# Kernel optimization log

Hardware: AMD Instinct MI355X
Metric: run time of the kernel (lower is better)

## Reference

```python
import jax, jax.numpy as jnp
import numpy as np

K_SIZE = 3            # kernel_size
PAD = K_SIZE // 2     # zero padding on each side
EPS = 1e-5            # torch layer_norm default eps


def setup_inputs() -> dict:
    key = jax.random.key(0)
    ks = jax.random.split(key, 9)
    B, C, H, W = 4, 256, 64, 64
    Cout = 256
    sc = 1.0 / np.sqrt(C)
    return {
        "x":  jax.random.normal(ks[0], (B, C, H, W), dtype=jnp.float32),
        "Wq": jax.random.normal(ks[1], (C, C), dtype=jnp.float32) * sc,
        "bq": jax.random.normal(ks[2], (C,), dtype=jnp.float32) * 0.02,
        "Wk": jax.random.normal(ks[3], (C, C), dtype=jnp.float32) * sc,
        "bk": jax.random.normal(ks[4], (C,), dtype=jnp.float32) * 0.02,
        "Wv": jax.random.normal(ks[5], (C, C), dtype=jnp.float32) * sc,
        "bv": jax.random.normal(ks[6], (C,), dtype=jnp.float32) * 0.02,
        "Wo": jax.random.normal(ks[7], (C, Cout), dtype=jnp.float32) * sc,
        "bo": jax.random.normal(ks[8], (Cout,), dtype=jnp.float32) * 0.02,
    }


def _forward(x, Wq, bq, Wk, bk, Wv, bv, Wo, bo):
    B, C, H, W = x.shape
    # F.layer_norm(x, [H, W]): normalize over last two dims per (b, c), no affine
    mean = jnp.mean(x, axis=(2, 3), keepdims=True)
    var = jnp.var(x, axis=(2, 3), keepdims=True)
    xn = (x - mean) * jax.lax.rsqrt(var + EPS)
    # zero pad spatial dims
    p = jnp.pad(xn, ((0, 0), (0, 0), (PAD, PAD), (PAD, PAD)))
    # channels-last for per-pixel linears
    p = jnp.transpose(p, (0, 2, 3, 1))          # [B, Hp, Wp, C]
    xc = jnp.transpose(xn, (0, 2, 3, 1))        # [B, H,  W,  C] (window centers)
    scale = jnp.asarray(C, x.dtype) ** -0.5     # depth_scale = C**-0.5
    q = (xc @ Wq + bq) * scale                  # [B, H, W, C] (center-token query)
    kf = p @ Wk + bk                            # [B, Hp, Wp, C]
    vf = p @ Wv + bv
    # gather the kk=9 shifted views -> window tokens per pixel
    Kw = jnp.stack([kf[:, dh:dh + H, dw:dw + W, :]
                    for dh in range(K_SIZE) for dw in range(K_SIZE)], axis=3)  # [B,H,W,kk,C]
    Vw = jnp.stack([vf[:, dh:dh + H, dw:dw + W, :]
                    for dh in range(K_SIZE) for dw in range(K_SIZE)], axis=3)
    logits = jnp.einsum('bhwc,bhwnc->bhwn', q, Kw)     # [B, H, W, kk]
    attn = jax.nn.softmax(logits, axis=-1)
    ctx = jnp.einsum('bhwn,bhwnc->bhwc', attn, Vw)     # [B, H, W, C]
    out = ctx @ Wo + bo                                # [B, H, W, Cout]
    return jnp.transpose(out, (0, 3, 1, 2))            # [B, Cout, H, W]


def reference(x, Wq, bq, Wk, bk, Wv, bv, Wo, bo):
    return _forward(x, Wq, bq, Wk, bk, Wv, bv, Wo, bo)
```

## Files before the change

### kernel.cpp

```cpp
#include <hip/hip_runtime.h>
#include <hip/hip_bf16.h>
#include <stdint.h>

typedef __bf16 bf16x8 __attribute__((ext_vector_type(8)));
typedef float f32x4 __attribute__((ext_vector_type(4)));

#define KDIM 256
#define MB 4608
#define MTOT 18432
#define QKVS 768

__device__ __forceinline__ float b2f(ushort u){
    union { float f; uint32_t i; } x; x.i = ((uint32_t)u) << 16; return x.f;
}
__device__ __forceinline__ ushort f2b(float f){
    uint32_t u = __float_as_uint(f);
    uint32_t r = (u + 0x7fffu + ((u >> 16) & 1u)) >> 16;
    return (ushort)r;
}

__global__ __launch_bounds__(256)
void ln_fuse(const float* __restrict__ x, ushort* __restrict__ xt,
             float* __restrict__ psum, float* __restrict__ psum2){
    __shared__ ushort sh[128 * 68];
    __shared__ float ssum[16 * 132], ssum2[16 * 132];
    const int bid = blockIdx.x;
    const int b = bid >> 7, rem = bid & 127, h = rem >> 1, ch = (rem & 1) * 128;
    const int tid = threadIdx.x;
    const int csub = tid >> 4, w4 = tid & 15;
#pragma unroll
    for (int i = 0; i < 8; ++i){
        int c = csub + 16 * i;
        float4 v = *(const float4*)(x + ((size_t)(b * 256 + ch + c)) * 4096
                                      + h * 64 + w4 * 4);
        ushort4 u; u.x = f2b(v.x); u.y = f2b(v.y); u.z = f2b(v.z); u.w = f2b(v.w);
        *(ushort4*)&sh[c * 68 + w4 * 4] = u;
        ssum [w4 * 132 + c] = v.x + v.y + v.z + v.w;
        ssum2[w4 * 132 + c] = v.x * v.x + v.y * v.y + v.z * v.z + v.w * v.w;
    }
    __syncthreads();
    if (tid < 128){
        float S = 0.f, S2 = 0.f;
#pragma unroll
        for (int j = 0; j < 16; ++j){ S += ssum[j * 132 + tid]; S2 += ssum2[j * 132 + tid]; }
        psum [(b * 64 + h) * 256 + ch + tid] = S;
        psum2[(b * 64 + h) * 256 + ch + tid] = S2;
    }
    const int c16 = tid & 15, w16 = tid >> 4;
#pragma unroll
    for (int p = 0; p < 4; ++p){
        int w = p * 16 + w16;
        union { ushort u[8]; uint4 v; } r;
#pragma unroll
        for (int j = 0; j < 8; ++j) r.u[j] = sh[(c16 * 8 + j) * 68 + w];
        size_t row = (size_t)b * MB + (size_t)(h + 1) * 66 + (w + 1);
        *(uint4*)(xt + row * 256 + ch + c16 * 8) = r.v;
    }
}

__global__ __launch_bounds__(256)
void prep2(const float* __restrict__ Wq, const float* __restrict__ bq,
           const float* __restrict__ Wk, const float* __restrict__ bk,
           const float* __restrict__ Wv, const float* __restrict__ bv,
           const float* __restrict__ Wo,
           const float* __restrict__ psum, const float* __restrict__ psum2,
           ushort* __restrict__ wtq, ushort* __restrict__ wot,
           float* __restrict__ biasp, ushort* __restrict__ xt){
    __shared__ float shW[32 * 33];
    __shared__ float shS[8 * 32], shS2[8 * 32], shRV[4 * 32], shM[256];
    const int bid = blockIdx.x, tid = threadIdx.x;
    if (bid < 192){
        int mat = bid / 64, tile = bid % 64;
        int ti = tile & 7, tj = tile >> 3;
        {
            int kk = tid & 31, idx = tid >> 5;
            int b = idx >> 1, h0 = (idx & 1) * 32;
            float S = 0.f, S2 = 0.f;
            for (int r = 0; r < 32; ++r){
                int off = (b * 64 + h0 + r) * 256 + tj * 32 + kk;
                S += psum[off]; S2 += psum2[off];
            }
            shS[idx * 32 + kk] = S; shS2[idx * 32 + kk] = S2;
        }
        __syncthreads();
        if (tid < 128){
            int b = tid >> 5, kk = tid & 31;
            float S  = shS [(b * 2) * 32 + kk] + shS [(b * 2 + 1) * 32 + kk];
            float S2 = shS2[(b * 2) * 32 + kk] + shS2[(b * 2 + 1) * 32 + kk];
            float m = S * (1.f / 4096.f);
            float v = S2 * (1.f / 4096.f) - m * m;
            shRV[b * 32 + kk] = rsqrtf(v + 1e-5f);
        }
        const float* src = (mat == 0) ? Wq : (mat == 1) ? Wk : Wv;
        float qs = (mat == 0) ? 0.0625f : 1.0f;
        int tx = tid & 31, ty = tid >> 5;
#pragma unroll
        for (int i = 0; i < 4; ++i)
            shW[(ty + i * 8) * 33 + tx] =
                src[(size_t)(tj * 32 + ty + i * 8) * 256 + ti * 32 + tx] * qs;
        __syncthreads();
#pragma unroll
        for (int b = 0; b < 4; ++b){
            float rv = shRV[b * 32 + tx];
#pragma unroll
            for (int i = 0; i < 4; ++i){
                int n = mat * 256 + ti * 32 + ty + i * 8;
                wtq[((size_t)b * 768 + n) * 256 + tj * 32 + tx] =
                    f2b(shW[tx * 33 + ty + i * 8] * rv);
            }
        }
    } else if (bid < 256){
        int tile = bid - 192;
        int ti = tile & 7, tj = tile >> 3;
        int tx = tid & 31, ty = tid >> 5;
#pragma unroll
        for (int i = 0; i < 4; ++i)
            shW[(ty + i * 8) * 33 + tx] =
                Wo[(size_t)(tj * 32 + ty + i * 8) * 256 + ti * 32 + tx];
        __syncthreads();
#pragma unroll
        for (int i = 0; i < 4; ++i)
            wot[(size_t)(ti * 32 + ty + i * 8) * 256 + tj * 32 + tx] =
                f2b(shW[tx * 33 + ty + i * 8]);
    } else if (bid < 268){
        int t = bid - 256;
        int b = t / 3, mat = t % 3;
        float S = 0.f, S2 = 0.f;
        for (int h = 0; h < 64; ++h){
            S += psum[(b * 64 + h) * 256 + tid]; S2 += psum2[(b * 64 + h) * 256 + tid];
        }
        float m = S * (1.f / 4096.f);
        float v = S2 * (1.f / 4096.f) - m * m;
        shM[tid] = m * rsqrtf(v + 1e-5f);
        __syncthreads();
        const float* W  = (mat == 0) ? Wq : (mat == 1) ? Wk : Wv;
        const float* bb = (mat == 0) ? bq : (mat == 1) ? bk : bv;
        float qs = (mat == 0) ? 0.0625f : 1.0f;
        float acc = 0.f;
        for (int c = 0; c < 256; ++c)
            acc += shM[c] * W[(size_t)c * 256 + tid];
        biasp[b * 768 + mat * 256 + tid] = (bb[tid] - acc) * qs;
    } else {
        int t = bid - 268;
        int b = t / 16, seg = t % 16;
        float S = 0.f;
        for (int h = 0; h < 64; ++h) S += psum[(b * 64 + h) * 256 + tid];
        ushort mb = f2b(S * (1.f / 4096.f));
        for (int r = 0; r < 32; ++r){
            int j = seg * 32 + r;
            int row;
            if (j < 260){
                int h66, w66;
                if (j < 66)       { h66 = 0;       w66 = j; }
                else if (j < 132) { h66 = 65;      w66 = j - 66; }
                else if (j < 196) { h66 = j - 131; w66 = 0; }
                else              { h66 = j - 195; w66 = 65; }
                row = h66 * 66 + w66;
            } else row = 4356 + (j - 260);
            xt[((size_t)b * MB + row) * 256 + tid] = mb;
        }
    }
}

__global__ __launch_bounds__(512, 1)
void gemm_qkv(const ushort* __restrict__ X, const ushort* __restrict__ Y,
              const float* __restrict__ bias, ushort* __restrict__ zb){
    __shared__ ushort ldsA[2][256 * 64];
    __shared__ ushort ldsB[2][256 * 64];
    const int tid  = threadIdx.x;
    const int lane = tid & 63;
    const int wid  = tid >> 6;
    const int wm   = wid >> 2;
    const int wn   = wid & 3;
    const int id    = blockIdx.x;
    const int mtile = id % 72, ntile = id / 72;
    const int x0 = mtile * 256, y0 = ntile * 256;
    const int bsel = x0 / MB;
    const ushort* Yb   = Y + ((size_t)bsel * QKVS + y0) * 256;
    const float* biasb = bias + bsel * 768;

    auto stage = [&](int buf, int k0){
#pragma unroll
        for (int i = 0; i < 4; ++i){
            int f   = i * 512 + tid;
            int row = f >> 3, cp = f & 7;
            int cs  = cp ^ (row & 7);
            const ushort* ga = X  + (size_t)(x0 + row) * KDIM + k0 + cs * 8;
            const ushort* gb = Yb + (size_t)row        * KDIM + k0 + cs * 8;
            __builtin_amdgcn_global_load_lds(
                (const __attribute__((address_space(1))) void*)ga,
                (__attribute__((address_space(3))) void*)&ldsA[buf][f * 8], 16, 0, 0);
            __builtin_amdgcn_global_load_lds(
                (const __attribute__((address_space(1))) void*)gb,
                (__attribute__((address_space(3))) void*)&ldsB[buf][f * 8], 16, 0, 0);
        }
    };

    f32x4 acc[8][4];
#pragma unroll
    for (int i = 0; i < 8; ++i)
#pragma unroll
        for (int j = 0; j < 4; ++j) acc[i][j] = f32x4{0.f, 0.f, 0.f, 0.f};

    stage(0, 0);
    stage(1, 64);
#pragma unroll
    for (int t = 0; t < 4; ++t){
        if (t < 3) asm volatile("s_waitcnt vmcnt(8)" ::: "memory");
        else       asm volatile("s_waitcnt vmcnt(0)" ::: "memory");
        __builtin_amdgcn_sched_barrier(0);
        __builtin_amdgcn_s_barrier();
        __builtin_amdgcn_sched_barrier(0);
        const int buf = t & 1;
        __builtin_amdgcn_s_setprio(1);
#pragma unroll
        for (int kk = 0; kk < 2; ++kk){
            bf16x8 af[8], bf[4];
#pragma unroll
            for (int fm = 0; fm < 8; ++fm){
                int r = wm * 128 + fm * 16 + (lane & 15);
                int c = kk * 4 + (lane >> 4);
                af[fm] = *(const bf16x8*)&ldsA[buf][(r * 8 + (c ^ (r & 7))) * 8];
            }
#pragma unroll
            for (int fn = 0; fn < 4; ++fn){
                int r = wn * 64 + fn * 16 + (lane & 15);
                int c = kk * 4 + (lane >> 4);
                bf[fn] = *(const bf16x8*)&ldsB[buf][(r * 8 + (c ^ (r & 7))) * 8];
            }
#pragma unroll
            for (int fm = 0; fm < 8; ++fm)
#pragma unroll
                for (int fn = 0; fn < 4; ++fn)
                    acc[fm][fn] = __builtin_amdgcn_mfma_f32_16x16x32_bf16(
                        af[fm], bf[fn], acc[fm][fn], 0, 0, 0);
        }
        __builtin_amdgcn_s_setprio(0);
        __builtin_amdgcn_sched_barrier(0);
        __builtin_amdgcn_s_barrier();
        __builtin_amdgcn_sched_barrier(0);
        if (t < 2) stage(t & 1, (t + 2) * 64);
    }

#pragma unroll
    for (int fm = 0; fm < 8; ++fm){
#pragma unroll
        for (int fn = 0; fn < 4; ++fn){
            int xr = x0 + wm * 128 + fm * 16 + ((lane >> 4) << 2);
            int yc = y0 + wn * 64 + fn * 16 + (lane & 15);
            float bv = biasb[yc];
#pragma unroll
            for (int r = 0; r < 4; ++r)
                zb[(size_t)(xr + r) * QKVS + yc] = f2b(acc[fm][fn][r] + bv);
        }
    }
}

__global__ __launch_bounds__(256, 2)
void gemm_out(const ushort* __restrict__ X, const ushort* __restrict__ Y,
              const float* __restrict__ bias, float* __restrict__ zf){
    __shared__ ushort ldsX[2][128 * 64];
    __shared__ ushort ldsY[2][128 * 64];
    const int tid  = threadIdx.x;
    const int lane = tid & 63;
    const int wid  = tid >> 6;
    const int wm   = wid >> 1, wn = wid & 1;
    const int x0   = blockIdx.x * 128, y0 = blockIdx.y * 128;

    auto stage = [&](int buf, int k0){
#pragma unroll
        for (int i = 0; i < 4; ++i){
            int f   = i * 256 + tid;
            int row = f >> 3, cp = f & 7;
            int cs  = cp ^ (row & 7);
            const ushort* gx = X + (size_t)(x0 + row) * KDIM + k0 + cs * 8;
            const ushort* gy = Y + (size_t)(y0 + row) * KDIM + k0 + cs * 8;
            __builtin_amdgcn_global_load_lds(
                (const __attribute__((address_space(1))) void*)gx,
                (__attribute__((address_space(3))) void*)&ldsX[buf][f * 8], 16, 0, 0);
            __builtin_amdgcn_global_load_lds(
                (const __attribute__((address_space(1))) void*)gy,
                (__attribute__((address_space(3))) void*)&ldsY[buf][f * 8], 16, 0, 0);
        }
    };

    f32x4 acc[4][4];
#pragma unroll
    for (int i = 0; i < 4; ++i)
#pragma unroll
        for (int j = 0; j < 4; ++j) acc[i][j] = f32x4{0.f, 0.f, 0.f, 0.f};

    stage(0, 0);
    int buf = 0;
    for (int t = 0; t < 4; ++t){
        __syncthreads();
        if (t < 3) stage(buf ^ 1, (t + 1) * 64);
#pragma unroll
        for (int kk = 0; kk < 2; ++kk){
            bf16x8 xa[4], yb[4];
#pragma unroll
            for (int fm = 0; fm < 4; ++fm){
                int r = wm * 64 + fm * 16 + (lane & 15);
                int c = kk * 4 + (lane >> 4);
                xa[fm] = *(const bf16x8*)&ldsX[buf][(r * 8 + (c ^ (r & 7))) * 8];
            }
#pragma unroll
            for (int fn = 0; fn < 4; ++fn){
                int r = wn * 64 + fn * 16 + (lane & 15);
                int c = kk * 4 + (lane >> 4);
                yb[fn] = *(const bf16x8*)&ldsY[buf][(r * 8 + (c ^ (r & 7))) * 8];
            }
#pragma unroll
            for (int fm = 0; fm < 4; ++fm)
#pragma unroll
                for (int fn = 0; fn < 4; ++fn)
                    acc[fm][fn] = __builtin_amdgcn_mfma_f32_16x16x32_bf16(
                        xa[fm], yb[fn], acc[fm][fn], 0, 0, 0);
        }
        buf ^= 1;
    }

#pragma unroll
    for (int fm = 0; fm < 4; ++fm){
#pragma unroll
        for (int fn = 0; fn < 4; ++fn){
            int xr = x0 + wm * 64 + fm * 16 + ((lane >> 4) << 2);
            int yc = y0 + wn * 64 + fn * 16 + (lane & 15);
            int bpix = yc >> 12, hw = yc & 4095;
#pragma unroll
            for (int r = 0; r < 4; ++r){
                int ch = xr + r;
                zf[((size_t)(bpix * 256 + ch)) * 4096 + hw] =
                    acc[fm][fn][r] + bias[ch];
            }
        }
    }
}

__global__ __launch_bounds__(256)
void attn_win(const ushort* __restrict__ qkv, ushort* __restrict__ ctx){
    int pix  = blockIdx.x * 4 + (threadIdx.x >> 6);
    int lane = threadIdx.x & 63;
    int b = pix >> 12, hw = pix & 4095;
    int h = hw >> 6, w = hw & 63;
    size_t base = (size_t)b * MB;
    size_t crow = base + (size_t)(h + 1) * 66 + (w + 1);

    ushort4 q4 = *(const ushort4*)(qkv + crow * QKVS + lane * 4);
    float q0 = b2f(q4.x), q1 = b2f(q4.y), q2 = b2f(q4.z), q3 = b2f(q4.w);

    float lg[9];
    size_t rows[9];
#pragma unroll
    for (int n = 0; n < 9; ++n){
        int dh = n / 3, dw = n % 3;
        size_t row = base + (size_t)(h + dh) * 66 + (w + dw);
        rows[n] = row;
        ushort4 k4 = *(const ushort4*)(qkv + row * QKVS + 256 + lane * 4);
        float d = q0 * b2f(k4.x) + q1 * b2f(k4.y) + q2 * b2f(k4.z) + q3 * b2f(k4.w);
#pragma unroll
        for (int off = 32; off; off >>= 1) d += __shfl_xor(d, off);
        lg[n] = d;
    }
    float m = lg[0];
#pragma unroll
    for (int n = 1; n < 9; ++n) m = fmaxf(m, lg[n]);
    float e[9], s = 0.f;
#pragma unroll
    for (int n = 0; n < 9; ++n){ e[n] = __expf(lg[n] - m); s += e[n]; }
    float inv = 1.f / s;

    float c0 = 0.f, c1 = 0.f, c2 = 0.f, c3 = 0.f;
#pragma unroll
    for (int n = 0; n < 9; ++n){
        float a = e[n] * inv;
        ushort4 v4 = *(const ushort4*)(qkv + rows[n] * QKVS + 512 + lane * 4);
        c0 += a * b2f(v4.x); c1 += a * b2f(v4.y);
        c2 += a * b2f(v4.z); c3 += a * b2f(v4.w);
    }
    ushort4 o; o.x = f2b(c0); o.y = f2b(c1); o.z = f2b(c2); o.w = f2b(c3);
    *(ushort4*)(ctx + (size_t)pix * 256 + lane * 4) = o;
}

extern "C" void kernel_launch(void* const* d_in, const int* in_sizes, int n_in,
                              void* d_out, int out_size, void* d_ws, size_t ws_size,
                              hipStream_t stream){
    const float* x  = (const float*)d_in[0];
    const float* Wq = (const float*)d_in[1];
    const float* bq = (const float*)d_in[2];
    const float* Wk = (const float*)d_in[3];
    const float* bk = (const float*)d_in[4];
    const float* Wv = (const float*)d_in[5];
    const float* bv = (const float*)d_in[6];
    const float* Wo = (const float*)d_in[7];
    const float* bo = (const float*)d_in[8];
    float* out = (float*)d_out;

    char* ws = (char*)d_ws;
    ushort* wtq    = (ushort*)(ws);
    ushort* wot    = (ushort*)(ws + 1572864);
    float*  biasp  = (float*) (ws + 1703936);
    float*  psum   = (float*) (ws + 1716224);
    float*  psum2  = (float*) (ws + 1978368);
    ushort* xt     = (ushort*)(ws + 2240512);
    ushort* qkv    = (ushort*)(ws + 11677696);
    ushort* ctx    = (ushort*)(ws + 39989248);

    ln_fuse<<<512, 256, 0, stream>>>(x, xt, psum, psum2);
    prep2<<<332, 256, 0, stream>>>(Wq, bq, Wk, bk, Wv, bv, Wo,
                                   psum, psum2, wtq, wot, biasp, xt);

    gemm_qkv<<<216, 512, 0, stream>>>(xt, wtq, biasp, qkv);

    attn_win<<<4096, 256, 0, stream>>>(qkv, ctx);

    dim3 g2(2, 128);
    gemm_out<<<g2, 256, 0, stream>>>(wot, ctx, bo, out);
}
```

Before: 59.28 us.

## Fuse windowed attention with output projection GEMM per image row

Merges the attention kernel and the output-projection GEMM into one kernel. Each block handles one image row: it computes 64 pixels of context into LDS and then multiplies by Wo straight from global memory, writing the NCHW output. This drops the ctx round trip through global memory and one launch. In exchange the grid shrinks to 256 blocks of 512 threads, and the Wo operand is no longer staged through LDS.

```diff
diff --git a/kernel.cpp b/kernel.cpp
--- a/kernel.cpp
+++ b/kernel.cpp
@@ -256,130 +256,96 @@
     }
 }
 
-__global__ __launch_bounds__(256, 2)
-void gemm_out(const ushort* __restrict__ X, const ushort* __restrict__ Y,
-              const float* __restrict__ bias, float* __restrict__ zf){
-    __shared__ ushort ldsX[2][128 * 64];
-    __shared__ ushort ldsY[2][128 * 64];
-    const int tid  = threadIdx.x;
-    const int lane = tid & 63;
-    const int wid  = tid >> 6;
-    const int wm   = wid >> 1, wn = wid & 1;
-    const int x0   = blockIdx.x * 128, y0 = blockIdx.y * 128;
-
-    auto stage = [&](int buf, int k0){
-#pragma unroll
-        for (int i = 0; i < 4; ++i){
-            int f   = i * 256 + tid;
-            int row = f >> 3, cp = f & 7;
-            int cs  = cp ^ (row & 7);
-            const ushort* gx = X + (size_t)(x0 + row) * KDIM + k0 + cs * 8;
-            const ushort* gy = Y + (size_t)(y0 + row) * KDIM + k0 + cs * 8;
-            __builtin_amdgcn_global_load_lds(
-                (const __attribute__((address_space(1))) void*)gx,
-                (__attribute__((address_space(3))) void*)&ldsX[buf][f * 8], 16, 0, 0);
-            __builtin_amdgcn_global_load_lds(
-                (const __attribute__((address_space(1))) void*)gy,
-                (__attribute__((address_space(3))) void*)&ldsY[buf][f * 8], 16, 0, 0);
-        }
-    };
-
-    f32x4 acc[4][4];
-#pragma unroll
-    for (int i = 0; i < 4; ++i)
-#pragma unroll
-        for (int j = 0; j < 4; ++j) acc[i][j] = f32x4{0.f, 0.f, 0.f, 0.f};
-
-    stage(0, 0);
-    int buf = 0;
-    for (int t = 0; t < 4; ++t){
-        __syncthreads();
-        if (t < 3) stage(buf ^ 1, (t + 1) * 64);
-#pragma unroll
-        for (int kk = 0; kk < 2; ++kk){
-            bf16x8 xa[4], yb[4];
-#pragma unroll
-            for (int fm = 0; fm < 4; ++fm){
-                int r = wm * 64 + fm * 16 + (lane & 15);
-                int c = kk * 4 + (lane >> 4);
-                xa[fm] = *(const bf16x8*)&ldsX[buf][(r * 8 + (c ^ (r & 7))) * 8];
-            }
-#pragma unroll
-            for (int fn = 0; fn < 4; ++fn){
-                int r = wn * 64 + fn * 16 + (lane & 15);
-                int c = kk * 4 + (lane >> 4);
-                yb[fn] = *(const bf16x8*)&ldsY[buf][(r * 8 + (c ^ (r & 7))) * 8];
-            }
-#pragma unroll
-            for (int fm = 0; fm < 4; ++fm)
-#pragma unroll
-                for (int fn = 0; fn < 4; ++fn)
-                    acc[fm][fn] = __builtin_amdgcn_mfma_f32_16x16x32_bf16(
-                        xa[fm], yb[fn], acc[fm][fn], 0, 0, 0);
-        }
-        buf ^= 1;
+__global__ __launch_bounds__(512, 1)
+void attn_out(const ushort* __restrict__ qkv, const ushort* __restrict__ wot,
+              const float* __restrict__ bo, float* __restrict__ out){
+    __shared__ ushort ctx[64 * 256];
+    const int tid = threadIdx.x, lane = tid & 63, wid = tid >> 6;
+    const int b = blockIdx.x >> 6, h = blockIdx.x & 63;
+    const uint base = (uint)b * MB;
+
+#pragma unroll 1
+    for (int j = 0; j < 8; ++j){
+        const int w = wid * 8 + j;
+        uint crow = base + (uint)(h + 1) * 66 + (w + 1);
+        ushort4 q4 = *(const ushort4*)(qkv + (size_t)crow * QKVS + lane * 4);
+        float q0 = b2f(q4.x), q1 = b2f(q4.y), q2 = b2f(q4.z), q3 = b2f(q4.w);
+
+        float lg[9];
+        uint rows[9];
+#pragma unroll
+        for (int n = 0; n < 9; ++n){
+            int dh = n / 3, dw = n % 3;
+            uint row = base + (uint)(h + dh) * 66 + (w + dw);
+            rows[n] = row;
+            ushort4 k4 = *(const ushort4*)(qkv + (size_t)row * QKVS + 256 + lane * 4);
+            float d = q0 * b2f(k4.x) + q1 * b2f(k4.y) + q2 * b2f(k4.z) + q3 * b2f(k4.w);
+#pragma unroll
+            for (int off = 32; off; off >>= 1) d += __shfl_xor(d, off);
+            lg[n] = d;
+        }
+        float m = lg[0];
+#pragma unroll
+        for (int n = 1; n < 9; ++n) m = fmaxf(m, lg[n]);
+        float e[9], s = 0.f;
+#pragma unroll
+        for (int n = 0; n < 9; ++n){ e[n] = __expf(lg[n] - m); s += e[n]; }
+        float inv = 1.f / s;
+
+        float c0 = 0.f, c1 = 0.f, c2 = 0.f, c3 = 0.f;
+#pragma unroll
+        for (int n = 0; n < 9; ++n){
+            float a = e[n] * inv;
+            ushort4 v4 = *(const ushort4*)(qkv + (size_t)rows[n] * QKVS + 512 + lane * 4);
+            c0 += a * b2f(v4.x); c1 += a * b2f(v4.y);
+            c2 += a * b2f(v4.z); c3 += a * b2f(v4.w);
+        }
+        ushort4 o; o.x = f2b(c0); o.y = f2b(c1); o.z = f2b(c2); o.w = f2b(c3);
+        *(ushort4*)&ctx[w * 256 + (((lane >> 1) ^ (w & 7)) * 8) + (lane & 1) * 4] = o;
+    }
+    __syncthreads();
+
+    const int wmi = wid >> 1, wni = wid & 1;
+    f32x4 acc[4][2];
+#pragma unroll
+    for (int i = 0; i < 4; ++i){ acc[i][0] = f32x4{0,0,0,0}; acc[i][1] = f32x4{0,0,0,0}; }
+
+#pragma unroll
+    for (int kk = 0; kk < 8; ++kk){
+        bf16x8 af[4], bf[2];
+        const int c = kk * 4 + (lane >> 4);
+#pragma unroll
+        for (int fm = 0; fm < 4; ++fm){
+            int r = wmi * 64 + fm * 16 + (lane & 15);
+            af[fm] = *(const bf16x8*)(wot + (size_t)r * 256 + c * 8);
+        }
+#pragma unroll
+        for (int fn = 0; fn < 2; ++fn){
+            int p = wni * 32 + fn * 16 + (lane & 15);
+            bf[fn] = *(const bf16x8*)&ctx[p * 256 + (c ^ (p & 7)) * 8];
+        }
+#pragma unroll
+        for (int fm = 0; fm < 4; ++fm)
+#pragma unroll
+            for (int fn = 0; fn < 2; ++fn)
+                acc[fm][fn] = __builtin_amdgcn_mfma_f32_16x16x32_bf16(
+                    af[fm], bf[fn], acc[fm][fn], 0, 0, 0);
     }
 
 #pragma unroll
     for (int fm = 0; fm < 4; ++fm){
 #pragma unroll
-        for (int fn = 0; fn < 4; ++fn){
-            int xr = x0 + wm * 64 + fm * 16 + ((lane >> 4) << 2);
-            int yc = y0 + wn * 64 + fn * 16 + (lane & 15);
-            int bpix = yc >> 12, hw = yc & 4095;
+        for (int fn = 0; fn < 2; ++fn){
+            int ch0  = wmi * 64 + fm * 16 + ((lane >> 4) << 2);
+            int wpix = wni * 32 + fn * 16 + (lane & 15);
 #pragma unroll
             for (int r = 0; r < 4; ++r){
-                int ch = xr + r;
-                zf[((size_t)(bpix * 256 + ch)) * 4096 + hw] =
-                    acc[fm][fn][r] + bias[ch];
-            }
-        }
-    }
-}
-
-__global__ __launch_bounds__(256)
-void attn_win(const ushort* __restrict__ qkv, ushort* __restrict__ ctx){
-    int pix  = blockIdx.x * 4 + (threadIdx.x >> 6);
-    int lane = threadIdx.x & 63;
-    int b = pix >> 12, hw = pix & 4095;
-    int h = hw >> 6, w = hw & 63;
-    size_t base = (size_t)b * MB;
-    size_t crow = base + (size_t)(h + 1) * 66 + (w + 1);
-
-    ushort4 q4 = *(const ushort4*)(qkv + crow * QKVS + lane * 4);
-    float q0 = b2f(q4.x), q1 = b2f(q4.y), q2 = b2f(q4.z), q3 = b2f(q4.w);
-
-    float lg[9];
-    size_t rows[9];
-#pragma unroll
-    for (int n = 0; n < 9; ++n){
-        int dh = n / 3, dw = n % 3;
-        size_t row = base + (size_t)(h + dh) * 66 + (w + dw);
-        rows[n] = row;
-        ushort4 k4 = *(const ushort4*)(qkv + row * QKVS + 256 + lane * 4);
-        float d = q0 * b2f(k4.x) + q1 * b2f(k4.y) + q2 * b2f(k4.z) + q3 * b2f(k4.w);
-#pragma unroll
-        for (int off = 32; off; off >>= 1) d += __shfl_xor(d, off);
-        lg[n] = d;
-    }
-    float m = lg[0];
-#pragma unroll
-    for (int n = 1; n < 9; ++n) m = fmaxf(m, lg[n]);
-    float e[9], s = 0.f;
-#pragma unroll
-    for (int n = 0; n < 9; ++n){ e[n] = __expf(lg[n] - m); s += e[n]; }
-    float inv = 1.f / s;
-
-    float c0 = 0.f, c1 = 0.f, c2 = 0.f, c3 = 0.f;
-#pragma unroll
-    for (int n = 0; n < 9; ++n){
-        float a = e[n] * inv;
-        ushort4 v4 = *(const ushort4*)(qkv + rows[n] * QKVS + 512 + lane * 4);
-        c0 += a * b2f(v4.x); c1 += a * b2f(v4.y);
-        c2 += a * b2f(v4.z); c3 += a * b2f(v4.w);
-    }
-    ushort4 o; o.x = f2b(c0); o.y = f2b(c1); o.z = f2b(c2); o.w = f2b(c3);
-    *(ushort4*)(ctx + (size_t)pix * 256 + lane * 4) = o;
+                int ch = ch0 + r;
+                out[((size_t)(b * 256 + ch)) * 4096 + h * 64 + wpix] =
+                    acc[fm][fn][r] + bo[ch];
+            }
+        }
+    }
 }
 
 extern "C" void kernel_launch(void* const* d_in, const int* in_sizes, int n_in,
@@ -404,7 +370,6 @@
     float*  psum2  = (float*) (ws + 1978368);
     ushort* xt     = (ushort*)(ws + 2240512);
     ushort* qkv    = (ushort*)(ws + 11677696);
-    ushort* ctx    = (ushort*)(ws + 39989248);
 
     ln_fuse<<<512, 256, 0, stream>>>(x, xt, psum, psum2);
     prep2<<<332, 256, 0, stream>>>(Wq, bq, Wk, bk, Wv, bv, Wo,
@@ -412,8 +377,5 @@
 
     gemm_qkv<<<216, 512, 0, stream>>>(xt, wtq, biasp, qkv);
 
-    attn_win<<<4096, 256, 0, stream>>>(qkv, ctx);
-
-    dim3 g2(2, 128);
-    gemm_out<<<g2, 256, 0, stream>>>(wot, ctx, bo, out);
-}
+    attn_out<<<256, 512, 0, stream>>>(qkv, wot, bo, out);
+}
```

New measurement: 82.06 us. 1.38x slower.

## Drop padded pixel layout; handle window borders via shared pad row

Applied to the files above, without the earlier changes.

The normalized input is now stored unpadded (16384 rows instead of 18432), so the QKV GEMM skips the padded border rows. Out-of-bounds window neighbours in the attention kernel point at a single extra row holding the K/V values a padded pixel would produce: bias only, which is exact because the input is mean-centered before the weight product. The QKV GEMM is also retiled from 256x256 tiles with 512 threads to 128x128 tiles with 256 threads and two blocks per CU. Its hand-tuned waitcnt/setprio pipeline is replaced by a simpler __syncthreads double buffer, which may expose more load latency.

```diff
diff --git a/kernel.cpp b/kernel.cpp
--- a/kernel.cpp
+++ b/kernel.cpp
@@ -6,8 +6,7 @@
 typedef float f32x4 __attribute__((ext_vector_type(4)));
 
 #define KDIM 256
-#define MB 4608
-#define MTOT 18432
+#define NPIX 16384
 #define QKVS 768
 
 __device__ __forceinline__ float b2f(ushort u){
@@ -53,7 +52,7 @@
         union { ushort u[8]; uint4 v; } r;
 #pragma unroll
         for (int j = 0; j < 8; ++j) r.u[j] = sh[(c16 * 8 + j) * 68 + w];
-        size_t row = (size_t)b * MB + (size_t)(h + 1) * 66 + (w + 1);
+        size_t row = (size_t)(b * 4096 + h * 64 + w);
         *(uint4*)(xt + row * 256 + ch + c16 * 8) = r.v;
     }
 }
@@ -65,7 +64,7 @@
            const float* __restrict__ Wo,
            const float* __restrict__ psum, const float* __restrict__ psum2,
            ushort* __restrict__ wtq, ushort* __restrict__ wot,
-           float* __restrict__ biasp, ushort* __restrict__ xt){
+           float* __restrict__ biasp, ushort* __restrict__ qkv){
     __shared__ float shW[32 * 33];
     __shared__ float shS[8 * 32], shS2[8 * 32], shRV[4 * 32], shM[256];
     const int bid = blockIdx.x, tid = threadIdx.x;
@@ -141,112 +140,85 @@
             acc += shM[c] * W[(size_t)c * 256 + tid];
         biasp[b * 768 + mat * 256 + tid] = (bb[tid] - acc) * qs;
     } else {
-        int t = bid - 268;
-        int b = t / 16, seg = t % 16;
-        float S = 0.f;
-        for (int h = 0; h < 64; ++h) S += psum[(b * 64 + h) * 256 + tid];
-        ushort mb = f2b(S * (1.f / 4096.f));
-        for (int r = 0; r < 32; ++r){
-            int j = seg * 32 + r;
-            int row;
-            if (j < 260){
-                int h66, w66;
-                if (j < 66)       { h66 = 0;       w66 = j; }
-                else if (j < 132) { h66 = 65;      w66 = j - 66; }
-                else if (j < 196) { h66 = j - 131; w66 = 0; }
-                else              { h66 = j - 195; w66 = 65; }
-                row = h66 * 66 + w66;
-            } else row = 4356 + (j - 260);
-            xt[((size_t)b * MB + row) * 256 + tid] = mb;
-        }
-    }
-}
-
-__global__ __launch_bounds__(512, 1)
+        ushort* pad = qkv + (size_t)NPIX * QKVS;
+        pad[tid]       = 0;
+        pad[256 + tid] = f2b(bk[tid]);
+        pad[512 + tid] = f2b(bv[tid]);
+    }
+}
+
+__global__ __launch_bounds__(256, 2)
 void gemm_qkv(const ushort* __restrict__ X, const ushort* __restrict__ Y,
               const float* __restrict__ bias, ushort* __restrict__ zb){
-    __shared__ ushort ldsA[2][256 * 64];
-    __shared__ ushort ldsB[2][256 * 64];
+    __shared__ ushort ldsX[2][128 * 64];
+    __shared__ ushort ldsY[2][128 * 64];
     const int tid  = threadIdx.x;
     const int lane = tid & 63;
     const int wid  = tid >> 6;
-    const int wm   = wid >> 2;
-    const int wn   = wid & 3;
-    const int id    = blockIdx.x;
-    const int mtile = id % 72, ntile = id / 72;
-    const int x0 = mtile * 256, y0 = ntile * 256;
-    const int bsel = x0 / MB;
-    const ushort* Yb   = Y + ((size_t)bsel * QKVS + y0) * 256;
-    const float* biasb = bias + bsel * 768;
+    const int wm   = wid >> 1, wn = wid & 1;
+    const int x0   = blockIdx.x * 128, y0 = blockIdx.y * 128;
+    const int bsel = x0 >> 12;
+    const ushort* Yb   = Y + (size_t)bsel * QKVS * 256;
+    const float* biasb = bias + bsel * QKVS;
 
     auto stage = [&](int buf, int k0){
 #pragma unroll
         for (int i = 0; i < 4; ++i){
-            int f   = i * 512 + tid;
+            int f   = i * 256 + tid;
             int row = f >> 3, cp = f & 7;
             int cs  = cp ^ (row & 7);
-            const ushort* ga = X  + (size_t)(x0 + row) * KDIM + k0 + cs * 8;
-            const ushort* gb = Yb + (size_t)row        * KDIM + k0 + cs * 8;
+            const ushort* gx = X  + (size_t)(x0 + row) * KDIM + k0 + cs * 8;
+            const ushort* gy = Yb + (size_t)(y0 + row) * KDIM + k0 + cs * 8;
             __builtin_amdgcn_global_load_lds(
-                (const __attribute__((address_space(1))) void*)ga,
-                (__attribute__((address_space(3))) void*)&ldsA[buf][f * 8], 16, 0, 0);
+                (const __attribute__((address_space(1))) void*)gx,
+                (__attribute__((address_space(3))) void*)&ldsX[buf][f * 8], 16, 0, 0);
             __builtin_amdgcn_global_load_lds(
-                (const __attribute__((address_space(1))) void*)gb,
-                (__attribute__((address_space(3))) void*)&ldsB[buf][f * 8], 16, 0, 0);
+                (const __attribute__((address_space(1))) void*)gy,
+                (__attribute__((address_space(3))) void*)&ldsY[buf][f * 8], 16, 0, 0);
         }
     };
 
-    f32x4 acc[8][4];
-#pragma unroll
-    for (int i = 0; i < 8; ++i)
+    f32x4 acc[4][4];
+#pragma unroll
+    for (int i = 0; i < 4; ++i)
 #pragma unroll
         for (int j = 0; j < 4; ++j) acc[i][j] = f32x4{0.f, 0.f, 0.f, 0.f};
 
     stage(0, 0);
-    stage(1, 64);
-#pragma unroll
+    int buf = 0;
     for (int t = 0; t < 4; ++t){
-        if (t < 3) asm volatile("s_waitcnt vmcnt(8)" ::: "memory");
-        else       asm volatile("s_waitcnt vmcnt(0)" ::: "memory");
-        __builtin_amdgcn_sched_barrier(0);
-        __builtin_amdgcn_s_barrier();
-        __builtin_amdgcn_sched_barrier(0);
-        const int buf = t & 1;
-        __builtin_amdgcn_s_setprio(1);
+        __syncthreads();
+        if (t < 3) stage(buf ^ 1, (t + 1) * 64);
 #pragma unroll
         for (int kk = 0; kk < 2; ++kk){
-            bf16x8 af[8], bf[4];
-#pragma unroll
-            for (int fm = 0; fm < 8; ++fm){
-                int r = wm * 128 + fm * 16 + (lane & 15);
+            bf16x8 xa[4], yb[4];
+#pragma unroll
+            for (int fm = 0; fm < 4; ++fm){
+                int r = wm * 64 + fm * 16 + (lane & 15);
                 int c = kk * 4 + (lane >> 4);
-                af[fm] = *(const bf16x8*)&ldsA[buf][(r * 8 + (c ^ (r & 7))) * 8];
+                xa[fm] = *(const bf16x8*)&ldsX[buf][(r * 8 + (c ^ (r & 7))) * 8];
             }
 #pragma unroll
             for (int fn = 0; fn < 4; ++fn){
                 int r = wn * 64 + fn * 16 + (lane & 15);
                 int c = kk * 4 + (lane >> 4);
-                bf[fn] = *(const bf16x8*)&ldsB[buf][(r * 8 + (c ^ (r & 7))) * 8];
-            }
-#pragma unroll
-            for (int fm = 0; fm < 8; ++fm)
+                yb[fn] = *(const bf16x8*)&ldsY[buf][(r * 8 + (c ^ (r & 7))) * 8];
+            }
+#pragma unroll
+            for (int fm = 0; fm < 4; ++fm)
 #pragma unroll
                 for (int fn = 0; fn < 4; ++fn)
                     acc[fm][fn] = __builtin_amdgcn_mfma_f32_16x16x32_bf16(
-                        af[fm], bf[fn], acc[fm][fn], 0, 0, 0);
-        }
-        __builtin_amdgcn_s_setprio(0);
-        __builtin_amdgcn_sched_barrier(0);
-        __builtin_amdgcn_s_barrier();
-        __builtin_amdgcn_sched_barrier(0);
-        if (t < 2) stage(t & 1, (t + 2) * 64);
-    }
-
-#pragma unroll
-    for (int fm = 0; fm < 8; ++fm){
+                        xa[fm], yb[fn], acc[fm][fn], 0, 0, 0);
+        }
+        buf ^= 1;
+    }
+
+#pragma unroll
+    for (int fm = 0; fm < 4; ++fm){
 #pragma unroll
         for (int fn = 0; fn < 4; ++fn){
-            int xr = x0 + wm * 128 + fm * 16 + ((lane >> 4) << 2);
+            int xr = x0 + wm * 64 + fm * 16 + ((lane >> 4) << 2);
             int yc = y0 + wn * 64 + fn * 16 + (lane & 15);
             float bv = biasb[yc];
 #pragma unroll
@@ -254,6 +226,50 @@
                 zb[(size_t)(xr + r) * QKVS + yc] = f2b(acc[fm][fn][r] + bv);
         }
     }
+}
+
+__global__ __launch_bounds__(256)
+void attn_win(const ushort* __restrict__ qkv, ushort* __restrict__ ctx){
+    int pix  = blockIdx.x * 4 + (threadIdx.x >> 6);
+    int lane = threadIdx.x & 63;
+    int b = pix >> 12, hw = pix & 4095;
+    int h = hw >> 6, w = hw & 63;
+    const size_t PADOFF = (size_t)NPIX * QKVS;
+
+    ushort4 q4 = *(const ushort4*)(qkv + (size_t)pix * QKVS + lane * 4);
+    float q0 = b2f(q4.x), q1 = b2f(q4.y), q2 = b2f(q4.z), q3 = b2f(q4.w);
+
+    float lg[9];
+    size_t roff[9];
+#pragma unroll
+    for (int n = 0; n < 9; ++n){
+        int nh = h + n / 3 - 1, nw = w + n % 3 - 1;
+        bool ok = ((unsigned)nh < 64u) & ((unsigned)nw < 64u);
+        roff[n] = ok ? (size_t)((b << 12) + (nh << 6) + nw) * QKVS : PADOFF;
+        ushort4 k4 = *(const ushort4*)(qkv + roff[n] + 256 + lane * 4);
+        float d = q0 * b2f(k4.x) + q1 * b2f(k4.y) + q2 * b2f(k4.z) + q3 * b2f(k4.w);
+#pragma unroll
+        for (int off = 32; off; off >>= 1) d += __shfl_xor(d, off);
+        lg[n] = d;
+    }
+    float m = lg[0];
+#pragma unroll
+    for (int n = 1; n < 9; ++n) m = fmaxf(m, lg[n]);
+    float e[9], s = 0.f;
+#pragma unroll
+    for (int n = 0; n < 9; ++n){ e[n] = __expf(lg[n] - m); s += e[n]; }
+    float inv = 1.f / s;
+
+    float c0 = 0.f, c1 = 0.f, c2 = 0.f, c3 = 0.f;
+#pragma unroll
+    for (int n = 0; n < 9; ++n){
+        float a = e[n] * inv;
+        ushort4 v4 = *(const ushort4*)(qkv + roff[n] + 512 + lane * 4);
+        c0 += a * b2f(v4.x); c1 += a * b2f(v4.y);
+        c2 += a * b2f(v4.z); c3 += a * b2f(v4.w);
+    }
+    ushort4 o; o.x = f2b(c0); o.y = f2b(c1); o.z = f2b(c2); o.w = f2b(c3);
+    *(ushort4*)(ctx + (size_t)pix * 256 + lane * 4) = o;
 }
 
 __global__ __launch_bounds__(256, 2)
@@ -335,51 +351,6 @@
             }
         }
     }
-}
-
-__global__ __launch_bounds__(256)
-void attn_win(const ushort* __restrict__ qkv, ushort* __restrict__ ctx){
-    int pix  = blockIdx.x * 4 + (threadIdx.x >> 6);
-    int lane = threadIdx.x & 63;
-    int b = pix >> 12, hw = pix & 4095;
-    int h = hw >> 6, w = hw & 63;
-    size_t base = (size_t)b * MB;
-    size_t crow = base + (size_t)(h + 1) * 66 + (w + 1);
-
-    ushort4 q4 = *(const ushort4*)(qkv + crow * QKVS + lane * 4);
-    float q0 = b2f(q4.x), q1 = b2f(q4.y), q2 = b2f(q4.z), q3 = b2f(q4.w);
-
-    float lg[9];
-    size_t rows[9];
-#pragma unroll
-    for (int n = 0; n < 9; ++n){
-        int dh = n / 3, dw = n % 3;
-        size_t row = base + (size_t)(h + dh) * 66 + (w + dw);
-        rows[n] = row;
-        ushort4 k4 = *(const ushort4*)(qkv + row * QKVS + 256 + lane * 4);
-        float d = q0 * b2f(k4.x) + q1 * b2f(k4.y) + q2 * b2f(k4.z) + q3 * b2f(k4.w);
-#pragma unroll
-        for (int off = 32; off; off >>= 1) d += __shfl_xor(d, off);
-        lg[n] = d;
-    }
-    float m = lg[0];
-#pragma unroll
-    for (int n = 1; n < 9; ++n) m = fmaxf(m, lg[n]);
-    float e[9], s = 0.f;
-#pragma unroll
-    for (int n = 0; n < 9; ++n){ e[n] = __expf(lg[n] - m); s += e[n]; }
-    float inv = 1.f / s;
-
-    float c0 = 0.f, c1 = 0.f, c2 = 0.f, c3 = 0.f;
-#pragma unroll
-    for (int n = 0; n < 9; ++n){
-        float a = e[n] * inv;
-        ushort4 v4 = *(const ushort4*)(qkv + rows[n] * QKVS + 512 + lane * 4);
-        c0 += a * b2f(v4.x); c1 += a * b2f(v4.y);
-        c2 += a * b2f(v4.z); c3 += a * b2f(v4.w);
-    }
-    ushort4 o; o.x = f2b(c0); o.y = f2b(c1); o.z = f2b(c2); o.w = f2b(c3);
-    *(ushort4*)(ctx + (size_t)pix * 256 + lane * 4) = o;
 }
 
 extern "C" void kernel_launch(void* const* d_in, const int* in_sizes, int n_in,
@@ -403,14 +374,15 @@
     float*  psum   = (float*) (ws + 1716224);
     float*  psum2  = (float*) (ws + 1978368);
     ushort* xt     = (ushort*)(ws + 2240512);
-    ushort* qkv    = (ushort*)(ws + 11677696);
-    ushort* ctx    = (ushort*)(ws + 39989248);
+    ushort* qkv    = (ushort*)(ws + 10629120);
+    ushort* ctx    = (ushort*)(ws + 35796480);
 
     ln_fuse<<<512, 256, 0, stream>>>(x, xt, psum, psum2);
-    prep2<<<332, 256, 0, stream>>>(Wq, bq, Wk, bk, Wv, bv, Wo,
-                                   psum, psum2, wtq, wot, biasp, xt);
-
-    gemm_qkv<<<216, 512, 0, stream>>>(xt, wtq, biasp, qkv);
+    prep2<<<269, 256, 0, stream>>>(Wq, bq, Wk, bk, Wv, bv, Wo,
+                                   psum, psum2, wtq, wot, biasp, qkv);
+
+    dim3 g1(128, 6);
+    gemm_qkv<<<g1, 256, 0, stream>>>(xt, wtq, biasp, qkv);
 
     attn_win<<<4096, 256, 0, stream>>>(qkv, ctx);
 
```

Result: slower. 63.48 us (+7.1%).

## Drop padded pixel layout; handle window borders with a shared pad row

Applied to the files above, without the earlier changes.

The QKV projection now runs only on the 64x64 real pixels instead of a 66x66 padded grid plus filler rows, which cuts GEMM tiles from 216 to 192 and removes the kernel that wrote padding rows into xt. Out-of-image window neighbours are redirected to one extra row holding the projection of the zero-padded input: zero for the unused q slot, bk and bv in the k and v slots. The attention kernel is rewritten so 16 lanes cover one pixel with 16 channels each, using wider 16-byte loads, shorter shuffle reductions and packed bf16 conversion. The costs are a per-neighbour bounds check and a layout change that every producer and consumer must agree on.

```diff
diff --git a/kernel.cpp b/kernel.cpp
--- a/kernel.cpp
+++ b/kernel.cpp
@@ -6,8 +6,7 @@
 typedef float f32x4 __attribute__((ext_vector_type(4)));
 
 #define KDIM 256
-#define MB 4608
-#define MTOT 18432
+#define NPIX 16384
 #define QKVS 768
 
 __device__ __forceinline__ float b2f(ushort u){
@@ -17,6 +16,15 @@
     uint32_t u = __float_as_uint(f);
     uint32_t r = (u + 0x7fffu + ((u >> 16) & 1u)) >> 16;
     return (ushort)r;
+}
+__device__ __forceinline__ void unpack2(uint d, float& lo, float& hi){
+    lo = __uint_as_float(d << 16);
+    hi = __uint_as_float(d & 0xffff0000u);
+}
+__device__ __forceinline__ uint cvtpk(float lo, float hi){
+    uint r;
+    asm volatile("v_cvt_pk_bf16_f32 %0, %1, %2" : "=v"(r) : "v"(lo), "v"(hi));
+    return r;
 }
 
 __global__ __launch_bounds__(256)
@@ -53,7 +61,7 @@
         union { ushort u[8]; uint4 v; } r;
 #pragma unroll
         for (int j = 0; j < 8; ++j) r.u[j] = sh[(c16 * 8 + j) * 68 + w];
-        size_t row = (size_t)b * MB + (size_t)(h + 1) * 66 + (w + 1);
+        size_t row = (size_t)(b * 4096 + h * 64 + w);
         *(uint4*)(xt + row * 256 + ch + c16 * 8) = r.v;
     }
 }
@@ -65,7 +73,7 @@
            const float* __restrict__ Wo,
            const float* __restrict__ psum, const float* __restrict__ psum2,
            ushort* __restrict__ wtq, ushort* __restrict__ wot,
-           float* __restrict__ biasp, ushort* __restrict__ xt){
+           float* __restrict__ biasp, ushort* __restrict__ qkv){
     __shared__ float shW[32 * 33];
     __shared__ float shS[8 * 32], shS2[8 * 32], shRV[4 * 32], shM[256];
     const int bid = blockIdx.x, tid = threadIdx.x;
@@ -141,24 +149,10 @@
             acc += shM[c] * W[(size_t)c * 256 + tid];
         biasp[b * 768 + mat * 256 + tid] = (bb[tid] - acc) * qs;
     } else {
-        int t = bid - 268;
-        int b = t / 16, seg = t % 16;
-        float S = 0.f;
-        for (int h = 0; h < 64; ++h) S += psum[(b * 64 + h) * 256 + tid];
-        ushort mb = f2b(S * (1.f / 4096.f));
-        for (int r = 0; r < 32; ++r){
-            int j = seg * 32 + r;
-            int row;
-            if (j < 260){
-                int h66, w66;
-                if (j < 66)       { h66 = 0;       w66 = j; }
-                else if (j < 132) { h66 = 65;      w66 = j - 66; }
-                else if (j < 196) { h66 = j - 131; w66 = 0; }
-                else              { h66 = j - 195; w66 = 65; }
-                row = h66 * 66 + w66;
-            } else row = 4356 + (j - 260);
-            xt[((size_t)b * MB + row) * 256 + tid] = mb;
-        }
+        ushort* pad = qkv + (size_t)NPIX * QKVS;
+        pad[tid]       = 0;
+        pad[256 + tid] = f2b(bk[tid]);
+        pad[512 + tid] = f2b(bv[tid]);
     }
 }
 
@@ -173,11 +167,11 @@
     const int wm   = wid >> 2;
     const int wn   = wid & 3;
     const int id    = blockIdx.x;
-    const int mtile = id % 72, ntile = id / 72;
+    const int mtile = id & 63, ntile = id >> 6;
     const int x0 = mtile * 256, y0 = ntile * 256;
-    const int bsel = x0 / MB;
+    const int bsel = x0 >> 12;
     const ushort* Yb   = Y + ((size_t)bsel * QKVS + y0) * 256;
-    const float* biasb = bias + bsel * 768;
+    const float* biasb = bias + bsel * QKVS;
 
     auto stage = [&](int buf, int k0){
 #pragma unroll
@@ -256,6 +250,83 @@
     }
 }
 
+__global__ __launch_bounds__(256)
+void attn_win(const ushort* __restrict__ qkv, ushort* __restrict__ ctx){
+    const int tid = threadIdx.x;
+    const int lane = tid & 63, wid = tid >> 6;
+    const int l16 = lane & 15, pg = lane >> 4;
+    const int pix = blockIdx.x * 16 + wid * 4 + pg;
+    const int b = pix >> 12, hw = pix & 4095;
+    const int h = hw >> 6, w = hw & 63;
+    const uint PADOFF = (uint)NPIX * QKVS;
+    const int cbase = l16 * 16;
+
+    const ushort* qp = qkv + (size_t)pix * QKVS + cbase;
+    uint4 qa = *(const uint4*)qp;
+    uint4 qb = *(const uint4*)(qp + 8);
+    float qf[16];
+    unpack2(qa.x, qf[0], qf[1]);  unpack2(qa.y, qf[2], qf[3]);
+    unpack2(qa.z, qf[4], qf[5]);  unpack2(qa.w, qf[6], qf[7]);
+    unpack2(qb.x, qf[8], qf[9]);  unpack2(qb.y, qf[10], qf[11]);
+    unpack2(qb.z, qf[12], qf[13]); unpack2(qb.w, qf[14], qf[15]);
+
+    float lg[9];
+    uint roff[9];
+#pragma unroll
+    for (int n = 0; n < 9; ++n){
+        int nh = h + n / 3 - 1, nw = w + n % 3 - 1;
+        bool ok = ((unsigned)nh < 64u) & ((unsigned)nw < 64u);
+        roff[n] = ok ? (uint)(((b << 12) + (nh << 6) + nw) * QKVS) : PADOFF;
+        const ushort* kp = qkv + roff[n] + 256 + cbase;
+        uint4 ka = *(const uint4*)kp;
+        uint4 kb = *(const uint4*)(kp + 8);
+        float kf[16];
+        unpack2(ka.x, kf[0], kf[1]);  unpack2(ka.y, kf[2], kf[3]);
+        unpack2(ka.z, kf[4], kf[5]);  unpack2(ka.w, kf[6], kf[7]);
+        unpack2(kb.x, kf[8], kf[9]);  unpack2(kb.y, kf[10], kf[11]);
+        unpack2(kb.z, kf[12], kf[13]); unpack2(kb.w, kf[14], kf[15]);
+        float d = 0.f;
+#pragma unroll
+        for (int j = 0; j < 16; ++j) d += qf[j] * kf[j];
+        d += __shfl_xor(d, 1); d += __shfl_xor(d, 2);
+        d += __shfl_xor(d, 4); d += __shfl_xor(d, 8);
+        lg[n] = d;
+    }
+    float m = lg[0];
+#pragma unroll
+    for (int n = 1; n < 9; ++n) m = fmaxf(m, lg[n]);
+    float e[9], s = 0.f;
+#pragma unroll
+    for (int n = 0; n < 9; ++n){ e[n] = __expf(lg[n] - m); s += e[n]; }
+    float inv = 1.f / s;
+
+    float c[16];
+#pragma unroll
+    for (int j = 0; j < 16; ++j) c[j] = 0.f;
+#pragma unroll
+    for (int n = 0; n < 9; ++n){
+        float a = e[n] * inv;
+        const ushort* vp = qkv + roff[n] + 512 + cbase;
+        uint4 va = *(const uint4*)vp;
+        uint4 vb = *(const uint4*)(vp + 8);
+        float vf[16];
+        unpack2(va.x, vf[0], vf[1]);  unpack2(va.y, vf[2], vf[3]);
+        unpack2(va.z, vf[4], vf[5]);  unpack2(va.w, vf[6], vf[7]);
+        unpack2(vb.x, vf[8], vf[9]);  unpack2(vb.y, vf[10], vf[11]);
+        unpack2(vb.z, vf[12], vf[13]); unpack2(vb.w, vf[14], vf[15]);
+#pragma unroll
+        for (int j = 0; j < 16; ++j) c[j] += a * vf[j];
+    }
+    uint4 oa, ob;
+    oa.x = cvtpk(c[0], c[1]);   oa.y = cvtpk(c[2], c[3]);
+    oa.z = cvtpk(c[4], c[5]);   oa.w = cvtpk(c[6], c[7]);
+    ob.x = cvtpk(c[8], c[9]);   ob.y = cvtpk(c[10], c[11]);
+    ob.z = cvtpk(c[12], c[13]); ob.w = cvtpk(c[14], c[15]);
+    ushort* op = ctx + (size_t)pix * 256 + cbase;
+    *(uint4*)op = oa;
+    *(uint4*)(op + 8) = ob;
+}
+
 __global__ __launch_bounds__(256, 2)
 void gemm_out(const ushort* __restrict__ X, const ushort* __restrict__ Y,
               const float* __restrict__ bias, float* __restrict__ zf){
@@ -335,51 +406,6 @@
             }
         }
     }
-}
-
-__global__ __launch_bounds__(256)
-void attn_win(const ushort* __restrict__ qkv, ushort* __restrict__ ctx){
-    int pix  = blockIdx.x * 4 + (threadIdx.x >> 6);
-    int lane = threadIdx.x & 63;
-    int b = pix >> 12, hw = pix & 4095;
-    int h = hw >> 6, w = hw & 63;
-    size_t base = (size_t)b * MB;
-    size_t crow = base + (size_t)(h + 1) * 66 + (w + 1);
-
-    ushort4 q4 = *(const ushort4*)(qkv + crow * QKVS + lane * 4);
-    float q0 = b2f(q4.x), q1 = b2f(q4.y), q2 = b2f(q4.z), q3 = b2f(q4.w);
-
-    float lg[9];
-    size_t rows[9];
-#pragma unroll
-    for (int n = 0; n < 9; ++n){
-        int dh = n / 3, dw = n % 3;
-        size_t row = base + (size_t)(h + dh) * 66 + (w + dw);
-        rows[n] = row;
-        ushort4 k4 = *(const ushort4*)(qkv + row * QKVS + 256 + lane * 4);
-        float d = q0 * b2f(k4.x) + q1 * b2f(k4.y) + q2 * b2f(k4.z) + q3 * b2f(k4.w);
-#pragma unroll
-        for (int off = 32; off; off >>= 1) d += __shfl_xor(d, off);
-        lg[n] = d;
-    }
-    float m = lg[0];
-#pragma unroll
-    for (int n = 1; n < 9; ++n) m = fmaxf(m, lg[n]);
-    float e[9], s = 0.f;
-#pragma unroll
-    for (int n = 0; n < 9; ++n){ e[n] = __expf(lg[n] - m); s += e[n]; }
-    float inv = 1.f / s;
-
-    float c0 = 0.f, c1 = 0.f, c2 = 0.f, c3 = 0.f;
-#pragma unroll
-    for (int n = 0; n < 9; ++n){
-        float a = e[n] * inv;
-        ushort4 v4 = *(const ushort4*)(qkv + rows[n] * QKVS + 512 + lane * 4);
-        c0 += a * b2f(v4.x); c1 += a * b2f(v4.y);
-        c2 += a * b2f(v4.z); c3 += a * b2f(v4.w);
-    }
-    ushort4 o; o.x = f2b(c0); o.y = f2b(c1); o.z = f2b(c2); o.w = f2b(c3);
-    *(ushort4*)(ctx + (size_t)pix * 256 + lane * 4) = o;
 }
 
 extern "C" void kernel_launch(void* const* d_in, const int* in_sizes, int n_in,
@@ -403,16 +429,16 @@
     float*  psum   = (float*) (ws + 1716224);
     float*  psum2  = (float*) (ws + 1978368);
     ushort* xt     = (ushort*)(ws + 2240512);
-    ushort* qkv    = (ushort*)(ws + 11677696);
-    ushort* ctx    = (ushort*)(ws + 39989248);
+    ushort* qkv    = (ushort*)(ws + 10629120);
+    ushort* ctx    = (ushort*)(ws + 35796480);
 
     ln_fuse<<<512, 256, 0, stream>>>(x, xt, psum, psum2);
-    prep2<<<332, 256, 0, stream>>>(Wq, bq, Wk, bk, Wv, bv, Wo,
-                                   psum, psum2, wtq, wot, biasp, xt);
-
-    gemm_qkv<<<216, 512, 0, stream>>>(xt, wtq, biasp, qkv);
-
-    attn_win<<<4096, 256, 0, stream>>>(qkv, ctx);
+    prep2<<<269, 256, 0, stream>>>(Wq, bq, Wk, bk, Wv, bv, Wo,
+                                   psum, psum2, wtq, wot, biasp, qkv);
+
+    gemm_qkv<<<192, 512, 0, stream>>>(xt, wtq, biasp, qkv);
+
+    attn_win<<<1024, 256, 0, stream>>>(qkv, ctx);
 
     dim3 g2(2, 128);
     gemm_out<<<g2, 256, 0, stream>>>(wot, ctx, bo, out);
```

After: 58.04 us. 1.02x faster.
